# Optimization experiments

Hardware: AMD Instinct MI355X
Metric: run time of the kernel (lower is better)

## Reference

```python
import jax, jax.numpy as jnp
import numpy as np

B, S, E, NH = 2, 2048, 1024, 8
DH = E // NH


def setup_inputs() -> dict:
    key = jax.random.key(0)
    ks = jax.random.split(key, 8)
    q = jax.random.normal(ks[0], (B, S, E), dtype=jnp.float32)
    k = jax.random.normal(ks[1], (B, S, E), dtype=jnp.float32)
    v = jax.random.normal(ks[2], (B, S, E), dtype=jnp.float32)
    # gate projections: Linear(3E -> NH)
    igate_w = jax.random.normal(ks[3], (NH, 3 * E), dtype=jnp.float32) * 0.02
    igate_b = jax.random.normal(ks[4], (NH,), dtype=jnp.float32) * 0.1
    fgate_w = jax.random.normal(ks[5], (NH, 3 * E), dtype=jnp.float32) * 0.02
    fgate_b = jnp.linspace(3.0, 6.0, NH, dtype=jnp.float32)  # bias_linspace_init_
    norm_weight = 1.0 + 0.01 * jax.random.normal(ks[6], (E,), dtype=jnp.float32)
    return {"q": q, "k": k, "v": v, "igate_w": igate_w, "igate_b": igate_b,
            "fgate_w": fgate_w, "fgate_b": fgate_b, "norm_weight": norm_weight}


def _mlstm_forward(q, k, v, igate_w, igate_b, fgate_w, fgate_b, norm_weight):
    eps = 1e-6
    gate_in = jnp.concatenate([q, k, v], axis=-1)            # (B,S,3E)
    i_pre = gate_in @ igate_w.T + igate_b                    # (B,S,NH)
    f_pre = gate_in @ fgate_w.T + fgate_b                    # (B,S,NH)
    i_pre = jnp.transpose(i_pre, (0, 2, 1))                  # (B,NH,S)
    f_pre = jnp.transpose(f_pre, (0, 2, 1))                  # (B,NH,S)

    qh = jnp.transpose(q.reshape(B, S, NH, DH), (0, 2, 1, 3))  # (B,NH,S,DH)
    kh = jnp.transpose(k.reshape(B, S, NH, DH), (0, 2, 1, 3))
    vh = jnp.transpose(v.reshape(B, S, NH, DH), (0, 2, 1, 3))

    # cumulative log forget gates; decay matrix D[i,j] = sum_{u=j+1..i} logsig(f_u) + i_pre[j]
    log_fg = jax.nn.log_sigmoid(f_pre)                       # (B,NH,S)
    cs = jnp.cumsum(log_fg, axis=-1)                         # (B,NH,S)
    diff = cs[:, :, :, None] - cs[:, :, None, :]             # (B,NH,S,S) = cs[i]-cs[j]
    causal = jnp.tril(jnp.ones((S, S), dtype=bool))
    log_fg_mat = jnp.where(causal, diff, -jnp.inf)
    log_D = log_fg_mat + i_pre[:, :, None, :]                # (B,NH,S,S)

    max_log_D = jnp.max(log_D, axis=-1, keepdims=True)       # rowwise stabilizer
    D = jnp.exp(log_D - max_log_D)

    qk = jnp.einsum("bhsd,bhtd->bhst", qh, kh / jnp.sqrt(jnp.float32(DH)))
    C = qk * D
    normalizer = jnp.maximum(jnp.abs(jnp.sum(C, axis=-1, keepdims=True)),
                             jnp.exp(-max_log_D))
    Cn = C / (normalizer + eps)
    h = jnp.einsum("bhst,bhtd->bhsd", Cn, vh)                # (B,NH,S,DH)

    # MultiHeadLayerNorm == group_norm(num_groups=NH): per-head, per-token over DH
    mu = jnp.mean(h, axis=-1, keepdims=True)
    var = jnp.var(h, axis=-1, keepdims=True)
    hn = (h - mu) / jnp.sqrt(var + 1e-5)
    hn = hn * norm_weight.reshape(NH, DH)[None, :, None, :]
    return jnp.transpose(hn, (0, 2, 1, 3)).reshape(B, S, E)


def reference(q, k, v, igate_w, igate_b, fgate_w, fgate_b, norm_weight):
    return _mlstm_forward(q, k, v, igate_w, igate_b, fgate_w, fgate_b, norm_weight)
```

## Files before the change

### kernel.cpp

```cpp
#include <hip/hip_runtime.h>
#include <hip/hip_bf16.h>
#include <math.h>

typedef __attribute__((ext_vector_type(8))) short bf16x8;
typedef __attribute__((ext_vector_type(16))) float f32x16;

namespace {
constexpr int kB = 2, kS = 2048, kE = 1024, kNH = 8, kDH = 128, kE3 = 3072;
constexpr float kLog2e = 1.4426950408889634f;
constexpr int kUnits = 27;
constexpr int kSplitPerBh = 20;
}

__device__ const int kOrder[kUnits] = {6,19,20,17,18,5,15,16,13,14,24,25,4,
                                       11,12,21,22,23,26,9,10,3,7,8,2,1,0};

__device__ __forceinline__ ushort f2bf(float x) {
  union { __hip_bfloat16 b; ushort u; } c; c.b = __float2bfloat16(x); return c.u;
}
__device__ __forceinline__ uint pk2(float a, float b) {
  return (uint)f2bf(a) | ((uint)f2bf(b) << 16);
}
__device__ __forceinline__ void gload16(const void* g, void* l) {
  __builtin_amdgcn_global_load_lds(
      (const __attribute__((address_space(1))) void*)g,
      (__attribute__((address_space(3))) void*)l, 16, 0, 0);
}
__device__ __forceinline__ f32x16 zero16() {
  f32x16 z;
#pragma unroll
  for (int i = 0; i < 16; ++i) z[i] = 0.f;
  return z;
}
union UB8 { uint4 u; bf16x8 f; };

__device__ __forceinline__ float butterfly64(float* acc, int lane) {
  int cur = 64;
#pragma unroll
  for (int lv = 0; lv < 6; ++lv) {
    const int bmask = 1 << lv;
    const int half = cur >> 1;
    const bool hi = (lane & bmask) != 0;
#pragma unroll
    for (int i = 0; i < 32; ++i) {
      if (i >= half) break;
      const float keep = hi ? acc[i + half] : acc[i];
      const float send = hi ? acc[i] : acc[i + half];
      acc[i] = keep + __shfl_xor(send, bmask);
    }
    cur = half;
  }
  return acc[0];
}

__global__ __launch_bounds__(256) void gates_kernel(
    const float* __restrict__ q, const float* __restrict__ k, const float* __restrict__ v,
    const float* __restrict__ iw, const float* __restrict__ ib,
    const float* __restrict__ fw, const float* __restrict__ fb,
    float* __restrict__ i_pre, float* __restrict__ f_pre) {
  const int tid = threadIdx.x;
  const int w = tid >> 6, lane = tid & 63;
  const int tokbase = blockIdx.x * 8;
  const int kh = w >> 1, gh = w & 1;
  const float* __restrict__ W = gh ? fw : iw;

  float acc[64];
#pragma unroll
  for (int i = 0; i < 64; ++i) acc[i] = 0.f;

  for (int step = 0; step < 24; ++step) {
    const int e = kh * 1536 + step * 64 + lane;
    const int seg = e >> 10;
    const int eo = e & 1023;
    const float* __restrict__ src = (seg == 0) ? q : (seg == 1) ? k : v;
    float gv[8];
#pragma unroll
    for (int t = 0; t < 8; ++t)
      gv[t] = src[(size_t)(tokbase + t) * kE + eo];
    float w8[8];
#pragma unroll
    for (int hh = 0; hh < 8; ++hh) w8[hh] = W[hh * kE3 + e];
#pragma unroll
    for (int t = 0; t < 8; ++t)
#pragma unroll
      for (int hh = 0; hh < 8; ++hh)
        acc[t * 8 + hh] += gv[t] * w8[hh];
  }
  const float r = butterfly64(acc, lane);
  const int a = ((lane & 1) << 5) | ((lane & 2) << 3) | ((lane & 4) << 1) |
                ((lane & 8) >> 1) | ((lane & 16) >> 3) | ((lane & 32) >> 5);
  __shared__ float red[4][64];
  red[w][a] = r;
  __syncthreads();
  if (tid < 128) {
    const int t = tid >> 4, g16 = tid & 15, hh = g16 & 7;
    const float val = (g16 < 8) ? red[0][t * 8 + hh] + red[2][t * 8 + hh]
                                : red[1][t * 8 + hh] + red[3][t * 8 + hh];
    const int token = tokbase + t;
    const int b = token >> 11, s = token & 2047;
    const size_t idx = ((size_t)(b * 8 + hh)) * kS + s;
    if (g16 < 8) i_pre[idx] = val + ib[hh];
    else         f_pre[idx] = val + fb[hh];
  }
}

__global__ __launch_bounds__(256) void scan_kernel(
    const float* __restrict__ i_pre, const float* __restrict__ f_pre,
    float* __restrict__ wt_out, float* __restrict__ M2_out, float* __restrict__ nfl_out,
    float* __restrict__ Cg) {
  const int bh = blockIdx.x;
  const int tid = threadIdx.x;
  const int w = tid >> 6, lane = tid & 63;
  __shared__ float wsum[4], wmax[4];
  const float* __restrict__ fp = f_pre + (size_t)bh * kS;
  const float* __restrict__ ip = i_pre + (size_t)bh * kS;
  const int s0 = tid * 8;

  const float4 fa = *reinterpret_cast<const float4*>(fp + s0);
  const float4 fb4 = *reinterpret_cast<const float4*>(fp + s0 + 4);
  float lf[8];
  {
    const float fv[8] = {fa.x, fa.y, fa.z, fa.w, fb4.x, fb4.y, fb4.z, fb4.w};
#pragma unroll
    for (int j = 0; j < 8; ++j)
      lf[j] = fminf(fv[j], 0.f) - log1pf(expf(-fabsf(fv[j])));
  }
  float run = 0.f, pcs[8];
#pragma unroll
  for (int j = 0; j < 8; ++j) { run += lf[j]; pcs[j] = run; }
  float x = run;
#pragma unroll
  for (int d = 1; d < 64; d <<= 1) {
    const float t = __shfl_up(x, d);
    if (lane >= d) x += t;
  }
  if (lane == 63) wsum[w] = x;
  __syncthreads();
  float woff = 0.f;
#pragma unroll
  for (int i = 0; i < 4; ++i) if (i < w) woff += wsum[i];
  const float csbase = woff + x - run;
  float cs[8];
#pragma unroll
  for (int j = 0; j < 8; ++j) cs[j] = csbase + pcs[j];

  const float4 ia = *reinterpret_cast<const float4*>(ip + s0);
  const float4 ib4 = *reinterpret_cast<const float4*>(ip + s0 + 4);
  float av[8];
  {
    const float iv[8] = {ia.x, ia.y, ia.z, ia.w, ib4.x, ib4.y, ib4.z, ib4.w};
#pragma unroll
    for (int j = 0; j < 8; ++j) av[j] = iv[j] - cs[j];
  }
  float rmax = -1e30f, pm[8];
#pragma unroll
  for (int j = 0; j < 8; ++j) { rmax = fmaxf(rmax, av[j]); pm[j] = rmax; }

  float tm = rmax;
  tm = fmaxf(tm, __shfl_xor(tm, 1));
  tm = fmaxf(tm, __shfl_xor(tm, 2));
  tm = fmaxf(tm, __shfl_xor(tm, 4));
  if ((lane & 7) == 0) Cg[bh * 32 + (tid >> 3)] = tm * kLog2e;

  float4 wtlo, wthi;
  wtlo.x = exp2f((av[0] - tm) * kLog2e); wtlo.y = exp2f((av[1] - tm) * kLog2e);
  wtlo.z = exp2f((av[2] - tm) * kLog2e); wtlo.w = exp2f((av[3] - tm) * kLog2e);
  wthi.x = exp2f((av[4] - tm) * kLog2e); wthi.y = exp2f((av[5] - tm) * kLog2e);
  wthi.z = exp2f((av[6] - tm) * kLog2e); wthi.w = exp2f((av[7] - tm) * kLog2e);

  float mi = rmax;
#pragma unroll
  for (int d = 1; d < 64; d <<= 1) {
    const float t = __shfl_up(mi, d);
    if (lane >= d) mi = fmaxf(mi, t);
  }
  if (lane == 63) wmax[w] = mi;
  float mexcl = __shfl_up(mi, 1);
  if (lane == 0) mexcl = -1e30f;
  __syncthreads();
  float wmoff = -1e30f;
#pragma unroll
  for (int i = 0; i < 4; ++i) if (i < w) wmoff = fmaxf(wmoff, wmax[i]);
  const float mbase = fmaxf(wmoff, mexcl);

  float M[8];
#pragma unroll
  for (int j = 0; j < 8; ++j) M[j] = fmaxf(mbase, pm[j]);
  float4 m2lo, m2hi, nflo, nfhi;
  m2lo.x = M[0] * kLog2e; m2lo.y = M[1] * kLog2e; m2lo.z = M[2] * kLog2e; m2lo.w = M[3] * kLog2e;
  m2hi.x = M[4] * kLog2e; m2hi.y = M[5] * kLog2e; m2hi.z = M[6] * kLog2e; m2hi.w = M[7] * kLog2e;
  nflo.x = expf(-(cs[0] + M[0])); nflo.y = expf(-(cs[1] + M[1]));
  nflo.z = expf(-(cs[2] + M[2])); nflo.w = expf(-(cs[3] + M[3]));
  nfhi.x = expf(-(cs[4] + M[4])); nfhi.y = expf(-(cs[5] + M[5]));
  nfhi.z = expf(-(cs[6] + M[6])); nfhi.w = expf(-(cs[7] + M[7]));
  const size_t o = (size_t)bh * kS + s0;
  *reinterpret_cast<float4*>(wt_out + o) = wtlo;
  *reinterpret_cast<float4*>(wt_out + o + 4) = wthi;
  *reinterpret_cast<float4*>(M2_out + o) = m2lo;
  *reinterpret_cast<float4*>(M2_out + o + 4) = m2hi;
  *reinterpret_cast<float4*>(nfl_out + o) = nflo;
  *reinterpret_cast<float4*>(nfl_out + o + 4) = nfhi;
}

__global__ __launch_bounds__(256) void convkv_kernel(
    const float* __restrict__ k, const float* __restrict__ v,
    ushort* __restrict__ Kb, ushort* __restrict__ Vtb) {
  const int b = blockIdx.y;
  const int s0 = blockIdx.x * 8;
  const int tid = threadIdx.x;
  const int w = tid >> 6, lane = tid & 63;
  __shared__ ushort Vst[8 * 1024];

#pragma unroll
  for (int t = 0; t < 2; ++t) {
    const int tokl = w * 2 + t;
    const int s = s0 + tokl;
    const size_t base = ((size_t)b * kS + s) * kE + lane * 16;
    const int hh = lane >> 3;

    const float4 k0 = *reinterpret_cast<const float4*>(k + base);
    const float4 k1 = *reinterpret_cast<const float4*>(k + base + 4);
    const float4 k2 = *reinterpret_cast<const float4*>(k + base + 8);
    const float4 k3 = *reinterpret_cast<const float4*>(k + base + 12);
    uint4 pa, pb;
    pa.x = pk2(k0.x, k0.y); pa.y = pk2(k0.z, k0.w);
    pa.z = pk2(k1.x, k1.y); pa.w = pk2(k1.z, k1.w);
    pb.x = pk2(k2.x, k2.y); pb.y = pk2(k2.z, k2.w);
    pb.z = pk2(k3.x, k3.y); pb.w = pk2(k3.z, k3.w);
    ushort* kd = Kb + ((size_t)(b * 8 + hh) * kS + s) * 128 + (lane & 7) * 16;
    *reinterpret_cast<uint4*>(kd) = pa;
    *reinterpret_cast<uint4*>(kd + 8) = pb;

    const float4 v0 = *reinterpret_cast<const float4*>(v + base);
    const float4 v1 = *reinterpret_cast<const float4*>(v + base + 4);
    const float4 v2 = *reinterpret_cast<const float4*>(v + base + 8);
    const float4 v3 = *reinterpret_cast<const float4*>(v + base + 12);
    uint4 va, vb4;
    va.x = pk2(v0.x, v0.y); va.y = pk2(v0.z, v0.w);
    va.z = pk2(v1.x, v1.y); va.w = pk2(v1.z, v1.w);
    vb4.x = pk2(v2.x, v2.y); vb4.y = pk2(v2.z, v2.w);
    vb4.z = pk2(v3.x, v3.y); vb4.w = pk2(v3.z, v3.w);
    const int cc0 = lane * 2, cc1 = lane * 2 + 1;
    *reinterpret_cast<uint4*>(reinterpret_cast<char*>(Vst) + tokl * 2048 +
                              ((cc0 ^ ((cc0 >> 3) & 7)) << 4)) = va;
    *reinterpret_cast<uint4*>(reinterpret_cast<char*>(Vst) + tokl * 2048 +
                              ((cc1 ^ ((cc1 >> 3) & 7)) << 4)) = vb4;
  }
  __syncthreads();

#pragma unroll
  for (int j = 0; j < 4; ++j) {
    const int e = j * 256 + tid;
    const int cc = e >> 3;
    const int off = ((cc ^ ((cc >> 3) & 7)) << 4) + (e & 7) * 2;
    uint tmp[4];
#pragma unroll
    for (int t2 = 0; t2 < 8; t2 += 2) {
      const ushort u0 = *reinterpret_cast<const ushort*>(
          reinterpret_cast<const char*>(Vst) + t2 * 2048 + off);
      const ushort u1 = *reinterpret_cast<const ushort*>(
          reinterpret_cast<const char*>(Vst) + (t2 + 1) * 2048 + off);
      tmp[t2 >> 1] = (uint)u0 | ((uint)u1 << 16);
    }
    uint4 o; o.x = tmp[0]; o.y = tmp[1]; o.z = tmp[2]; o.w = tmp[3];
    ushort* vd = Vtb + ((size_t)(b * 8 + (e >> 7)) * 128 + (e & 127)) * kS + s0;
    *reinterpret_cast<uint4*>(vd) = o;
  }
}

__global__ __launch_bounds__(256, 2) void attn_mfma_kernel(
    const float* __restrict__ qg, const ushort* __restrict__ Kb,
    const ushort* __restrict__ Vtb, const float* __restrict__ wt,
    const float* __restrict__ Cg, const float* __restrict__ M2,
    const float* __restrict__ nfl, const float* __restrict__ nw,
    float* __restrict__ out, float* __restrict__ ph, float* __restrict__ prs) {
  const int bh = blockIdx.y;
  const int b = bh >> 3, h = bh & 7;
  const int u = kOrder[blockIdx.x];
  int it, j0, j1, cid = -1;
  if (u <= 6) { it = u; const int T = 2 * it + 2; j0 = 0; j1 = T - 1; }
  else if (u <= 20) {
    const int s = u - 7; it = 7 + (s >> 1); const int ci = s & 1;
    const int T = 2 * it + 2;
    j0 = (T * ci) >> 1; j1 = ((T * (ci + 1)) >> 1) - 1;
    cid = bh * kSplitPerBh + (u - 7);
  } else {
    const int s = u - 21; it = 14 + (s >= 3 ? 1 : 0); const int ci = s - (s >= 3 ? 3 : 0);
    const int T = 2 * it + 2;
    j0 = (T * ci) / 3; j1 = (T * (ci + 1)) / 3 - 1;
    cid = bh * kSplitPerBh + (u - 7);
  }
  const int tid = threadIdx.x;
  const int w = tid >> 6, lane = tid & 63;
  const int l31 = lane & 31, hi = lane >> 5;
  const int row_w = it * 128 + w * 32;
  const int ig = row_w + l31;
  const size_t bhS = (size_t)bh * kS;

  __shared__ ushort Klds[2 * 64 * 128];
  __shared__ ushort Vlds[2 * 128 * 64];
  __shared__ float Wlds[2 * 64];
  __shared__ float rsx[4][32];

  const char* __restrict__ KgBase = reinterpret_cast<const char*>(Kb + bhS * 128);
  const char* __restrict__ VgBase = reinterpret_cast<const char*>(Vtb + (size_t)bh * 128 * kS);
  const char* __restrict__ WgBase = reinterpret_cast<const char*>(wt + bhS);

  bf16x8 qf[8];
  {
    const float scale = 0.08838834764831845f;
    const float* qrow = qg + ((size_t)b * kS + ig) * kE + h * kDH;
#pragma unroll
    for (int ks = 0; ks < 8; ++ks) {
      const int d0 = ks * 16 + hi * 8;
      const float4 lo = *reinterpret_cast<const float4*>(qrow + d0);
      const float4 hi4 = *reinterpret_cast<const float4*>(qrow + d0 + 4);
      UB8 f;
      f.u.x = pk2(lo.x * scale, lo.y * scale);
      f.u.y = pk2(lo.z * scale, lo.w * scale);
      f.u.z = pk2(hi4.x * scale, hi4.y * scale);
      f.u.w = pk2(hi4.z * scale, hi4.w * scale);
      qf[ks] = f.f;
    }
  }
  const float M2i = M2[bhS + ig];

  int koffG[4], voffG[4];
#pragma unroll
  for (int i = 0; i < 4; ++i) {
    const int L = tid * 16 + i * 4096;
    { const int j = L >> 8, c = (L >> 4) & 15;
      koffG[i] = j * 256 + ((c ^ (j & 15)) << 4); }
    { const int d = L >> 7, c = (L >> 4) & 7;
      voffG[i] = d * 4096 + ((c ^ (d & 7)) << 4); }
  }
  auto stage = [&](int buf, int jt) {
    const char* Kg = KgBase + (size_t)jt * 16384;
    const char* Vg = VgBase + (size_t)jt * 128;
    char* kl = reinterpret_cast<char*>(Klds) + buf * 16384 + tid * 16;
    char* vl = reinterpret_cast<char*>(Vlds) + buf * 16384 + tid * 16;
#pragma unroll
    for (int i = 0; i < 4; ++i) gload16(Kg + koffG[i], kl + i * 4096);
#pragma unroll
    for (int i = 0; i < 4; ++i) gload16(Vg + voffG[i], vl + i * 4096);
    if (tid < 16)
      gload16(WgBase + jt * 256 + tid * 16,
              reinterpret_cast<char*>(Wlds) + buf * 256 + tid * 16);
  };

  f32x16 hacc[4];
#pragma unroll
  for (int dc = 0; dc < 4; ++dc) hacc[dc] = zero16();
  float rs = 0.f;

  stage(0, j0);
  __syncthreads();

  for (int jt = j0; jt <= j1; ++jt) {
    const int cur = (jt - j0) & 1;
    if (jt < j1) stage(cur ^ 1, jt + 1);
    const int jlo = jt * 64;
    const bool v0 = (jlo <= row_w + 31);
    const bool v1 = (jlo + 32 <= row_w + 31);
    const bool fullmask = (jlo + 63 <= row_w);

    if (v0) {
      const float f = exp2f(Cg[bh * 32 + jt] - M2i);
      const char* kb = reinterpret_cast<const char*>(Klds) + cur * 16384;
      const char* vb = reinterpret_cast<const char*>(Vlds) + cur * 16384;
      const float* Wf = Wlds + cur * 64;
      const int ksw = (l31 & 15) << 4;

      f32x16 sacc0 = zero16(), sacc1 = zero16();
#pragma unroll
      for (int ks = 0; ks < 8; ++ks) {
        const int colb = 32 * ks + 16 * hi;
        const bf16x8 kf0 = *reinterpret_cast<const bf16x8*>(
            kb + l31 * 256 + (colb ^ ksw));
        sacc0 = __builtin_amdgcn_mfma_f32_32x32x16_bf16(kf0, qf[ks], sacc0, 0, 0, 0);
        if (v1) {
          const bf16x8 kf1 = *reinterpret_cast<const bf16x8*>(
              kb + (32 + l31) * 256 + (colb ^ ksw));
          sacc1 = __builtin_amdgcn_mfma_f32_32x32x16_bf16(kf1, qf[ks], sacc1, 0, 0, 0);
        }
      }

      uint pkw[2][8];
#pragma unroll
      for (int jc = 0; jc < 2; ++jc) {
        if (jc == 1 && !v1) break;
        const f32x16 sa = jc ? sacc1 : sacc0;
        float p[16];
#pragma unroll
        for (int r = 0; r < 16; ++r) {
          const int joff = jc * 32 + (r & 3) + 8 * (r >> 2) + 4 * hi;
          float val = sa[r] * (Wf[joff] * f);
          if (!fullmask) val = (jlo + joff <= ig) ? val : 0.f;
          rs += val; p[r] = val;
        }
#pragma unroll
        for (int q2 = 0; q2 < 8; ++q2) pkw[jc][q2] = pk2(p[2 * q2], p[2 * q2 + 1]);
      }

#pragma unroll
      for (int ks = 0; ks < 4; ++ks) {
        const int jc = ks >> 1, ks2 = ks & 1;
        if (jc == 1 && !v1) break;
        UB8 pf;
        pf.u.x = pkw[jc][ks2 * 4 + 0]; pf.u.y = pkw[jc][ks2 * 4 + 1];
        pf.u.z = pkw[jc][ks2 * 4 + 2]; pf.u.w = pkw[jc][ks2 * 4 + 3];
        const int colb = 64 * jc + 32 * ks2 + 8 * hi;
#pragma unroll
        for (int dc = 0; dc < 4; ++dc) {
          const int d = dc * 32 + l31;
          const char* vrow = vb + d * 128;
          const int sw = (d & 7) << 4;
          const uint2 a = *reinterpret_cast<const uint2*>(vrow + (colb ^ sw));
          const uint2 c = *reinterpret_cast<const uint2*>(vrow + ((colb + 16) ^ sw));
          UB8 vf; vf.u.x = a.x; vf.u.y = a.y; vf.u.z = c.x; vf.u.w = c.y;
          hacc[dc] = __builtin_amdgcn_mfma_f32_32x32x16_bf16(pf.f, vf.f, hacc[dc], 0, 0, 0);
        }
      }
    }
    __syncthreads();
  }

  const float rs_tot = rs + __shfl_xor(rs, 32);

  if (cid >= 0) {
    float* pb = ph + (size_t)cid * 16384;
#pragma unroll
    for (int dc = 0; dc < 4; ++dc)
#pragma unroll
      for (int r = 0; r < 16; ++r) {
        const int il = w * 32 + (r & 3) + 8 * (r >> 2) + 4 * hi;
        pb[il * 128 + dc * 32 + l31] = hacc[dc][r];
      }
    if (hi == 0) prs[cid * 128 + w * 32 + l31] = rs_tot;
    return;
  }

  if (hi == 0) rsx[w][l31] = rs_tot;
  float nwv[4];
#pragma unroll
  for (int dc = 0; dc < 4; ++dc) nwv[dc] = nw[h * kDH + dc * 32 + l31];
#pragma unroll
  for (int r = 0; r < 16; ++r) {
    const int imap = (r & 3) + 8 * (r >> 2) + 4 * hi;
    const float rsum = rsx[w][imap];
    const float nf = nfl[bhS + row_w + imap];
    const float inv = 1.f / (fmaxf(fabsf(rsum), nf) + 1e-6f);
    float hv[4];
    float s1 = 0.f, s2 = 0.f;
#pragma unroll
    for (int dc = 0; dc < 4; ++dc) {
      hv[dc] = hacc[dc][r] * inv;
      s1 += hv[dc]; s2 += hv[dc] * hv[dc];
    }
#pragma unroll
    for (int off = 1; off <= 16; off <<= 1) {
      s1 += __shfl_xor(s1, off);
      s2 += __shfl_xor(s2, off);
    }
    const float mu = s1 * (1.f / 128.f);
    const float var = s2 * (1.f / 128.f) - mu * mu;
    const float rstd = rsqrtf(var + 1e-5f);
    float* __restrict__ orow = out + ((size_t)b * kS + row_w + imap) * kE + h * kDH;
#pragma unroll
    for (int dc = 0; dc < 4; ++dc)
      orow[dc * 32 + l31] = (hv[dc] - mu) * rstd * nwv[dc];
  }
}

__global__ __launch_bounds__(256) void combine_kernel(
    const float* __restrict__ ph, const float* __restrict__ prs,
    const float* __restrict__ nfl, const float* __restrict__ nw,
    float* __restrict__ out) {
  const int blk = blockIdx.x;
  const int bh = blk / 9, ct = blk % 9;
  const int b = bh >> 3, h = bh & 7;
  const int it = 7 + ct;
  const int nc = (ct < 7) ? 2 : 3;
  const int cb0 = bh * kSplitPerBh + ((ct < 7) ? ct * 2 : 14 + (ct - 7) * 3);
  const int tid = threadIdx.x;
  __shared__ float sinv[128];
  if (tid < 128) {
    float rsum = 0.f;
    for (int c = 0; c < nc; ++c) rsum += prs[(cb0 + c) * 128 + tid];
    const float nf = nfl[(size_t)bh * kS + it * 128 + tid];
    sinv[tid] = 1.f / (fmaxf(fabsf(rsum), nf) + 1e-6f);
  }
  __syncthreads();
  for (int kk = 0; kk < 16; ++kk) {
    const int idx = kk * 256 + tid;
    const int row = idx >> 5, c4 = idx & 31;
    float ax = 0.f, ay = 0.f, az = 0.f, aw = 0.f;
    for (int c = 0; c < nc; ++c) {
      const float4 t = *reinterpret_cast<const float4*>(
          ph + (size_t)(cb0 + c) * 16384 + row * 128 + c4 * 4);
      ax += t.x; ay += t.y; az += t.z; aw += t.w;
    }
    const float inv = sinv[row];
    ax *= inv; ay *= inv; az *= inv; aw *= inv;
    float s1 = ax + ay + az + aw;
    float s2 = ax * ax + ay * ay + az * az + aw * aw;
#pragma unroll
    for (int off = 1; off <= 16; off <<= 1) {
      s1 += __shfl_xor(s1, off);
      s2 += __shfl_xor(s2, off);
    }
    const float mu = s1 * (1.f / 128.f);
    const float var = s2 * (1.f / 128.f) - mu * mu;
    const float rstd = rsqrtf(var + 1e-5f);
    const float4 nw4 = *reinterpret_cast<const float4*>(nw + h * kDH + c4 * 4);
    float4 o;
    o.x = (ax - mu) * rstd * nw4.x;
    o.y = (ay - mu) * rstd * nw4.y;
    o.z = (az - mu) * rstd * nw4.z;
    o.w = (aw - mu) * rstd * nw4.w;
    *reinterpret_cast<float4*>(
        out + ((size_t)b * kS + it * 128 + row) * kE + h * kDH + c4 * 4) = o;
  }
}

extern "C" void kernel_launch(void* const* d_in, const int* in_sizes, int n_in,
                              void* d_out, int out_size, void* d_ws, size_t ws_size,
                              hipStream_t stream) {
  const float* q  = (const float*)d_in[0];
  const float* k  = (const float*)d_in[1];
  const float* v  = (const float*)d_in[2];
  const float* iw = (const float*)d_in[3];
  const float* ib = (const float*)d_in[4];
  const float* fw = (const float*)d_in[5];
  const float* fb = (const float*)d_in[6];
  const float* nw = (const float*)d_in[7];
  float* out = (float*)d_out;

  char* ws = (char*)d_ws;
  const int BHS = kB * kNH * kS;
  float* i_pre = (float*)ws;
  float* f_pre = i_pre + BHS;
  float* wt    = i_pre + 2 * BHS;
  float* M2    = i_pre + 3 * BHS;
  float* nfl   = i_pre + 4 * BHS;
  float* Cg    = i_pre + 5 * BHS;
  ushort* Kb  = (ushort*)(ws + (size_t)(5 * BHS + 512) * 4);
  ushort* Vtb = Kb + (size_t)kB * kNH * kS * kDH;
  float* ph   = (float*)(Vtb + (size_t)kB * kNH * kS * kDH);
  float* prs  = ph + (size_t)320 * 128 * 128;

  gates_kernel<<<dim3(kB * kS / 8), dim3(256), 0, stream>>>(q, k, v, iw, ib, fw, fb,
                                                            i_pre, f_pre);
  scan_kernel<<<dim3(kB * kNH), dim3(256), 0, stream>>>(i_pre, f_pre, wt, M2, nfl, Cg);
  convkv_kernel<<<dim3(kS / 8, kB), dim3(256), 0, stream>>>(k, v, Kb, Vtb);
  attn_mfma_kernel<<<dim3(kUnits, kB * kNH), dim3(256), 0, stream>>>(
      q, Kb, Vtb, wt, Cg, M2, nfl, nw, out, ph, prs);
  combine_kernel<<<dim3(kB * kNH * 9), dim3(256), 0, stream>>>(ph, prs, nfl, nw, out);
}
```

Baseline: 118.4 us.

## Fuse K/V bf16 conversion into gate kernel and move per-tile weights to registers

Merges the convkv kernel into the gate-projection kernel, so one launch reads k and v once and emits both the bf16 K/Vt buffers and the gate pre-activations. In the attention kernel, the per-tile decay weights and Cg values are now loaded into registers and broadcast with shuffles instead of staged through LDS, and the row-sum exchange uses shuffles rather than shared memory. The attention grid is flattened to 1D with heads interleaved within each work unit, which changes the order in which blocks are dispatched. In exchange it adds many shuffles in the inner loop and makes the preprocessing kernel longer and heavier on registers.

```diff
diff --git a/kernel.cpp b/kernel.cpp
--- a/kernel.cpp
+++ b/kernel.cpp
@@ -53,17 +53,77 @@
   return acc[0];
 }
 
-__global__ __launch_bounds__(256) void gates_kernel(
+__global__ __launch_bounds__(256) void preproc_kernel(
     const float* __restrict__ q, const float* __restrict__ k, const float* __restrict__ v,
     const float* __restrict__ iw, const float* __restrict__ ib,
     const float* __restrict__ fw, const float* __restrict__ fb,
+    ushort* __restrict__ Kb, ushort* __restrict__ Vtb,
     float* __restrict__ i_pre, float* __restrict__ f_pre) {
+  const int b = blockIdx.y;
+  const int s0 = blockIdx.x * 8;
   const int tid = threadIdx.x;
   const int w = tid >> 6, lane = tid & 63;
-  const int tokbase = blockIdx.x * 8;
+  __shared__ ushort Vst[8 * 1024];
+
+#pragma unroll
+  for (int t = 0; t < 2; ++t) {
+    const int tokl = w * 2 + t;
+    const int s = s0 + tokl;
+    const size_t base = ((size_t)b * kS + s) * kE + lane * 16;
+    const int hh = lane >> 3;
+
+    const float4 k0 = *reinterpret_cast<const float4*>(k + base);
+    const float4 k1 = *reinterpret_cast<const float4*>(k + base + 4);
+    const float4 k2 = *reinterpret_cast<const float4*>(k + base + 8);
+    const float4 k3 = *reinterpret_cast<const float4*>(k + base + 12);
+    uint4 pa, pb;
+    pa.x = pk2(k0.x, k0.y); pa.y = pk2(k0.z, k0.w);
+    pa.z = pk2(k1.x, k1.y); pa.w = pk2(k1.z, k1.w);
+    pb.x = pk2(k2.x, k2.y); pb.y = pk2(k2.z, k2.w);
+    pb.z = pk2(k3.x, k3.y); pb.w = pk2(k3.z, k3.w);
+    ushort* kd = Kb + ((size_t)(b * 8 + hh) * kS + s) * 128 + (lane & 7) * 16;
+    *reinterpret_cast<uint4*>(kd) = pa;
+    *reinterpret_cast<uint4*>(kd + 8) = pb;
+
+    const float4 v0 = *reinterpret_cast<const float4*>(v + base);
+    const float4 v1 = *reinterpret_cast<const float4*>(v + base + 4);
+    const float4 v2 = *reinterpret_cast<const float4*>(v + base + 8);
+    const float4 v3 = *reinterpret_cast<const float4*>(v + base + 12);
+    uint4 va, vb4;
+    va.x = pk2(v0.x, v0.y); va.y = pk2(v0.z, v0.w);
+    va.z = pk2(v1.x, v1.y); va.w = pk2(v1.z, v1.w);
+    vb4.x = pk2(v2.x, v2.y); vb4.y = pk2(v2.z, v2.w);
+    vb4.z = pk2(v3.x, v3.y); vb4.w = pk2(v3.z, v3.w);
+    const int cc0 = lane * 2, cc1 = lane * 2 + 1;
+    *reinterpret_cast<uint4*>(reinterpret_cast<char*>(Vst) + tokl * 2048 +
+                              ((cc0 ^ ((cc0 >> 3) & 7)) << 4)) = va;
+    *reinterpret_cast<uint4*>(reinterpret_cast<char*>(Vst) + tokl * 2048 +
+                              ((cc1 ^ ((cc1 >> 3) & 7)) << 4)) = vb4;
+  }
+  __syncthreads();
+
+#pragma unroll
+  for (int j = 0; j < 4; ++j) {
+    const int e = j * 256 + tid;
+    const int cc = e >> 3;
+    const int off = ((cc ^ ((cc >> 3) & 7)) << 4) + (e & 7) * 2;
+    uint tmp[4];
+#pragma unroll
+    for (int t2 = 0; t2 < 8; t2 += 2) {
+      const ushort u0 = *reinterpret_cast<const ushort*>(
+          reinterpret_cast<const char*>(Vst) + t2 * 2048 + off);
+      const ushort u1 = *reinterpret_cast<const ushort*>(
+          reinterpret_cast<const char*>(Vst) + (t2 + 1) * 2048 + off);
+      tmp[t2 >> 1] = (uint)u0 | ((uint)u1 << 16);
+    }
+    uint4 o; o.x = tmp[0]; o.y = tmp[1]; o.z = tmp[2]; o.w = tmp[3];
+    ushort* vd = Vtb + ((size_t)(b * 8 + (e >> 7)) * 128 + (e & 127)) * kS + s0;
+    *reinterpret_cast<uint4*>(vd) = o;
+  }
+  __syncthreads();
+
   const int kh = w >> 1, gh = w & 1;
   const float* __restrict__ W = gh ? fw : iw;
-
   float acc[64];
 #pragma unroll
   for (int i = 0; i < 64; ++i) acc[i] = 0.f;
@@ -76,7 +136,7 @@
     float gv[8];
 #pragma unroll
     for (int t = 0; t < 8; ++t)
-      gv[t] = src[(size_t)(tokbase + t) * kE + eo];
+      gv[t] = src[((size_t)b * kS + s0 + t) * kE + eo];
     float w8[8];
 #pragma unroll
     for (int hh = 0; hh < 8; ++hh) w8[hh] = W[hh * kE3 + e];
@@ -89,16 +149,14 @@
   const float r = butterfly64(acc, lane);
   const int a = ((lane & 1) << 5) | ((lane & 2) << 3) | ((lane & 4) << 1) |
                 ((lane & 8) >> 1) | ((lane & 16) >> 3) | ((lane & 32) >> 5);
-  __shared__ float red[4][64];
-  red[w][a] = r;
+  float* red = reinterpret_cast<float*>(Vst);
+  red[w * 64 + a] = r;
   __syncthreads();
   if (tid < 128) {
     const int t = tid >> 4, g16 = tid & 15, hh = g16 & 7;
-    const float val = (g16 < 8) ? red[0][t * 8 + hh] + red[2][t * 8 + hh]
-                                : red[1][t * 8 + hh] + red[3][t * 8 + hh];
-    const int token = tokbase + t;
-    const int b = token >> 11, s = token & 2047;
-    const size_t idx = ((size_t)(b * 8 + hh)) * kS + s;
+    const float val = (g16 < 8) ? red[0 * 64 + t * 8 + hh] + red[2 * 64 + t * 8 + hh]
+                                : red[1 * 64 + t * 8 + hh] + red[3 * 64 + t * 8 + hh];
+    const size_t idx = ((size_t)(b * 8 + hh)) * kS + s0 + t;
     if (g16 < 8) i_pre[idx] = val + ib[hh];
     else         f_pre[idx] = val + fb[hh];
   }
@@ -202,81 +260,17 @@
   *reinterpret_cast<float4*>(nfl_out + o + 4) = nfhi;
 }
 
-__global__ __launch_bounds__(256) void convkv_kernel(
-    const float* __restrict__ k, const float* __restrict__ v,
-    ushort* __restrict__ Kb, ushort* __restrict__ Vtb) {
-  const int b = blockIdx.y;
-  const int s0 = blockIdx.x * 8;
-  const int tid = threadIdx.x;
-  const int w = tid >> 6, lane = tid & 63;
-  __shared__ ushort Vst[8 * 1024];
-
-#pragma unroll
-  for (int t = 0; t < 2; ++t) {
-    const int tokl = w * 2 + t;
-    const int s = s0 + tokl;
-    const size_t base = ((size_t)b * kS + s) * kE + lane * 16;
-    const int hh = lane >> 3;
-
-    const float4 k0 = *reinterpret_cast<const float4*>(k + base);
-    const float4 k1 = *reinterpret_cast<const float4*>(k + base + 4);
-    const float4 k2 = *reinterpret_cast<const float4*>(k + base + 8);
-    const float4 k3 = *reinterpret_cast<const float4*>(k + base + 12);
-    uint4 pa, pb;
-    pa.x = pk2(k0.x, k0.y); pa.y = pk2(k0.z, k0.w);
-    pa.z = pk2(k1.x, k1.y); pa.w = pk2(k1.z, k1.w);
-    pb.x = pk2(k2.x, k2.y); pb.y = pk2(k2.z, k2.w);
-    pb.z = pk2(k3.x, k3.y); pb.w = pk2(k3.z, k3.w);
-    ushort* kd = Kb + ((size_t)(b * 8 + hh) * kS + s) * 128 + (lane & 7) * 16;
-    *reinterpret_cast<uint4*>(kd) = pa;
-    *reinterpret_cast<uint4*>(kd + 8) = pb;
-
-    const float4 v0 = *reinterpret_cast<const float4*>(v + base);
-    const float4 v1 = *reinterpret_cast<const float4*>(v + base + 4);
-    const float4 v2 = *reinterpret_cast<const float4*>(v + base + 8);
-    const float4 v3 = *reinterpret_cast<const float4*>(v + base + 12);
-    uint4 va, vb4;
-    va.x = pk2(v0.x, v0.y); va.y = pk2(v0.z, v0.w);
-    va.z = pk2(v1.x, v1.y); va.w = pk2(v1.z, v1.w);
-    vb4.x = pk2(v2.x, v2.y); vb4.y = pk2(v2.z, v2.w);
-    vb4.z = pk2(v3.x, v3.y); vb4.w = pk2(v3.z, v3.w);
-    const int cc0 = lane * 2, cc1 = lane * 2 + 1;
-    *reinterpret_cast<uint4*>(reinterpret_cast<char*>(Vst) + tokl * 2048 +
-                              ((cc0 ^ ((cc0 >> 3) & 7)) << 4)) = va;
-    *reinterpret_cast<uint4*>(reinterpret_cast<char*>(Vst) + tokl * 2048 +
-                              ((cc1 ^ ((cc1 >> 3) & 7)) << 4)) = vb4;
-  }
-  __syncthreads();
-
-#pragma unroll
-  for (int j = 0; j < 4; ++j) {
-    const int e = j * 256 + tid;
-    const int cc = e >> 3;
-    const int off = ((cc ^ ((cc >> 3) & 7)) << 4) + (e & 7) * 2;
-    uint tmp[4];
-#pragma unroll
-    for (int t2 = 0; t2 < 8; t2 += 2) {
-      const ushort u0 = *reinterpret_cast<const ushort*>(
-          reinterpret_cast<const char*>(Vst) + t2 * 2048 + off);
-      const ushort u1 = *reinterpret_cast<const ushort*>(
-          reinterpret_cast<const char*>(Vst) + (t2 + 1) * 2048 + off);
-      tmp[t2 >> 1] = (uint)u0 | ((uint)u1 << 16);
-    }
-    uint4 o; o.x = tmp[0]; o.y = tmp[1]; o.z = tmp[2]; o.w = tmp[3];
-    ushort* vd = Vtb + ((size_t)(b * 8 + (e >> 7)) * 128 + (e & 127)) * kS + s0;
-    *reinterpret_cast<uint4*>(vd) = o;
-  }
-}
-
 __global__ __launch_bounds__(256, 2) void attn_mfma_kernel(
     const float* __restrict__ qg, const ushort* __restrict__ Kb,
     const ushort* __restrict__ Vtb, const float* __restrict__ wt,
     const float* __restrict__ Cg, const float* __restrict__ M2,
     const float* __restrict__ nfl, const float* __restrict__ nw,
     float* __restrict__ out, float* __restrict__ ph, float* __restrict__ prs) {
-  const int bh = blockIdx.y;
+  const int id = blockIdx.x;
+  const int r8 = id & 7, qq = id >> 3;
+  const int bh = r8 + 8 * (qq & 1);
+  const int u = kOrder[qq >> 1];
   const int b = bh >> 3, h = bh & 7;
-  const int u = kOrder[blockIdx.x];
   int it, j0, j1, cid = -1;
   if (u <= 6) { it = u; const int T = 2 * it + 2; j0 = 0; j1 = T - 1; }
   else if (u <= 20) {
@@ -299,12 +293,10 @@
 
   __shared__ ushort Klds[2 * 64 * 128];
   __shared__ ushort Vlds[2 * 128 * 64];
-  __shared__ float Wlds[2 * 64];
-  __shared__ float rsx[4][32];
 
   const char* __restrict__ KgBase = reinterpret_cast<const char*>(Kb + bhS * 128);
   const char* __restrict__ VgBase = reinterpret_cast<const char*>(Vtb + (size_t)bh * 128 * kS);
-  const char* __restrict__ WgBase = reinterpret_cast<const char*>(wt + bhS);
+  const float* __restrict__ wtb = wt + bhS;
 
   bf16x8 qf[8];
   {
@@ -324,6 +316,7 @@
     }
   }
   const float M2i = M2[bhS + ig];
+  const float cgreg = Cg[bh * 32 + l31];
 
   int koffG[4], voffG[4];
 #pragma unroll
@@ -343,9 +336,6 @@
     for (int i = 0; i < 4; ++i) gload16(Kg + koffG[i], kl + i * 4096);
 #pragma unroll
     for (int i = 0; i < 4; ++i) gload16(Vg + voffG[i], vl + i * 4096);
-    if (tid < 16)
-      gload16(WgBase + jt * 256 + tid * 16,
-              reinterpret_cast<char*>(Wlds) + buf * 256 + tid * 16);
   };
 
   f32x16 hacc[4];
@@ -353,22 +343,28 @@
   for (int dc = 0; dc < 4; ++dc) hacc[dc] = zero16();
   float rs = 0.f;
 
+  float wtc0 = wtb[j0 * 64 + l31];
+  float wtc1 = wtb[j0 * 64 + 32 + l31];
   stage(0, j0);
   __syncthreads();
 
   for (int jt = j0; jt <= j1; ++jt) {
     const int cur = (jt - j0) & 1;
-    if (jt < j1) stage(cur ^ 1, jt + 1);
+    float wtn0, wtn1;
+    if (jt < j1) {
+      stage(cur ^ 1, jt + 1);
+      wtn0 = wtb[(jt + 1) * 64 + l31];
+      wtn1 = wtb[(jt + 1) * 64 + 32 + l31];
+    }
     const int jlo = jt * 64;
     const bool v0 = (jlo <= row_w + 31);
     const bool v1 = (jlo + 32 <= row_w + 31);
     const bool fullmask = (jlo + 63 <= row_w);
 
     if (v0) {
-      const float f = exp2f(Cg[bh * 32 + jt] - M2i);
+      const float f = exp2f(__shfl(cgreg, jt) - M2i);
       const char* kb = reinterpret_cast<const char*>(Klds) + cur * 16384;
       const char* vb = reinterpret_cast<const char*>(Vlds) + cur * 16384;
-      const float* Wf = Wlds + cur * 64;
       const int ksw = (l31 & 15) << 4;
 
       f32x16 sacc0 = zero16(), sacc1 = zero16();
@@ -393,9 +389,10 @@
         float p[16];
 #pragma unroll
         for (int r = 0; r < 16; ++r) {
-          const int joff = jc * 32 + (r & 3) + 8 * (r >> 2) + 4 * hi;
-          float val = sa[r] * (Wf[joff] * f);
-          if (!fullmask) val = (jlo + joff <= ig) ? val : 0.f;
+          const int c = (r & 3) + 8 * (r >> 2);
+          const float wv = __shfl(jc ? wtc1 : wtc0, c + 4 * hi);
+          float val = sa[r] * (wv * f);
+          if (!fullmask) val = (jlo + jc * 32 + c + 4 * hi <= ig) ? val : 0.f;
           rs += val; p[r] = val;
         }
 #pragma unroll
@@ -423,6 +420,7 @@
       }
     }
     __syncthreads();
+    if (jt < j1) { wtc0 = wtn0; wtc1 = wtn1; }
   }
 
   const float rs_tot = rs + __shfl_xor(rs, 32);
@@ -440,14 +438,13 @@
     return;
   }
 
-  if (hi == 0) rsx[w][l31] = rs_tot;
   float nwv[4];
 #pragma unroll
   for (int dc = 0; dc < 4; ++dc) nwv[dc] = nw[h * kDH + dc * 32 + l31];
 #pragma unroll
   for (int r = 0; r < 16; ++r) {
     const int imap = (r & 3) + 8 * (r >> 2) + 4 * hi;
-    const float rsum = rsx[w][imap];
+    const float rsum = __shfl(rs_tot, imap);
     const float nf = nfl[bhS + row_w + imap];
     const float inv = 1.f / (fmaxf(fabsf(rsum), nf) + 1e-6f);
     float hv[4];
@@ -549,11 +546,10 @@
   float* ph   = (float*)(Vtb + (size_t)kB * kNH * kS * kDH);
   float* prs  = ph + (size_t)320 * 128 * 128;
 
-  gates_kernel<<<dim3(kB * kS / 8), dim3(256), 0, stream>>>(q, k, v, iw, ib, fw, fb,
-                                                            i_pre, f_pre);
+  preproc_kernel<<<dim3(kS / 8, kB), dim3(256), 0, stream>>>(
+      q, k, v, iw, ib, fw, fb, Kb, Vtb, i_pre, f_pre);
   scan_kernel<<<dim3(kB * kNH), dim3(256), 0, stream>>>(i_pre, f_pre, wt, M2, nfl, Cg);
-  convkv_kernel<<<dim3(kS / 8, kB), dim3(256), 0, stream>>>(k, v, Kb, Vtb);
-  attn_mfma_kernel<<<dim3(kUnits, kB * kNH), dim3(256), 0, stream>>>(
+  attn_mfma_kernel<<<dim3(kUnits * kB * kNH), dim3(256), 0, stream>>>(
       q, Kb, Vtb, wt, Cg, M2, nfl, nw, out, ph, prs);
   combine_kernel<<<dim3(kB * kNH * 9), dim3(256), 0, stream>>>(ph, prs, nfl, nw, out);
 }
```

Result: slower. 122.6 us (+3.5%).
